# Performance work log

Measured on AMD Instinct MI355X. Metric: run time of the kernel, lower is better.

Reference implementation:

```python
import jax, jax.numpy as jnp
import numpy as np

NUM_CLASSES = 2
THRESHOLD = 0.35
NEGPOS_RATIO = 3
VAR0, VAR1 = 0.1, 0.2
ALPHA = 1.0
B, P, G = 16, 131072, 64


def _iou(a, b):
    # a: [G,4] point-form gts, b: [P,4] point-form priors -> [G,P]
    tl = jnp.maximum(a[:, None, :2], b[None, :, :2])
    br = jnp.minimum(a[:, None, 2:], b[None, :, 2:])
    wh = jnp.clip(br - tl, 0.0)
    inter = wh[..., 0] * wh[..., 1]
    area_a = (a[:, 2] - a[:, 0]) * (a[:, 3] - a[:, 1])
    area_b = (b[:, 2] - b[:, 0]) * (b[:, 3] - b[:, 1])
    return inter / (area_a[:, None] + area_b[None, :] - inter)


def setup_inputs() -> dict:
    key = jax.random.key(0)
    k1, k2, k3, k4, k5, k6 = jax.random.split(key, 6)
    loc_preds = jax.random.normal(k1, (B, P, 4), jnp.float32)
    cls_preds = jax.random.normal(k2, (B, P, NUM_CLASSES), jnp.float32)
    # priors in center form [cx, cy, w, h]
    pcxy = jax.random.uniform(k3, (P, 2), jnp.float32)
    pwh = 0.02 + 0.15 * jax.random.uniform(k4, (P, 2), jnp.float32)
    priorbox = jnp.concatenate([pcxy, pwh], axis=1)
    # ground-truth boxes; stored as [y1,x1,y2,x2,label] so that the module's
    # column permutation [1,0,3,2] yields valid point-form [x1,y1,x2,y2]
    xy1 = 0.8 * jax.random.uniform(k5, (B, G, 2), jnp.float32)
    wh = 0.02 + 0.1 * jax.random.uniform(k6, (B, G, 2), jnp.float32)
    xy2 = xy1 + wh
    boxes_perm = jnp.stack([xy1[..., 1], xy1[..., 0], xy2[..., 1], xy2[..., 0]], axis=-1)
    labels = jnp.ones((B, G, 1), jnp.float32)  # single foreground class (face)
    targets = jnp.concatenate([boxes_perm, labels], axis=-1)
    return {"loc_preds": loc_preds, "cls_preds": cls_preds,
            "priorbox": priorbox, "targets": targets}


def _loss(loc_preds, cls_preds, priorbox, targets):
    priors_c = priorbox[: loc_preds.shape[1], :]
    priors_pt = jnp.concatenate(
        [priors_c[:, :2] - priors_c[:, 2:] / 2,
         priors_c[:, :2] + priors_c[:, 2:] / 2], axis=1)
    num_g = targets.shape[1]

    def match_one(t):
        gts = t[:, :4][:, jnp.array([1, 0, 3, 2])]  # -> point form [x1,y1,x2,y2]
        labels = t[:, 4]
        ov = _iou(gts, priors_pt)                    # [G,P]
        best_prior_idx = jnp.argmax(ov, axis=1)      # [G]
        bto = jnp.max(ov, axis=0)                    # [P] best gt overlap per prior
        bti = jnp.argmax(ov, axis=0)                 # [P]
        bto = bto.at[best_prior_idx].set(2.0)        # force best prior per gt
        bti = bti.at[best_prior_idx].set(jnp.arange(num_g))
        conf = jnp.where(bto < THRESHOLD, 0.0, labels[bti])
        m = gts[bti]                                 # [P,4] matched gt boxes
        g_cxcy = ((m[:, :2] + m[:, 2:]) / 2 - priors_c[:, :2]) / (VAR0 * priors_c[:, 2:])
        g_wh = jnp.log((m[:, 2:] - m[:, :2]) / priors_c[:, 2:]) / VAR1
        return conf, jnp.concatenate([g_cxcy, g_wh], axis=1)

    cls_batch, loc_batch = jax.vmap(match_one)(targets)
    cls_batch = jax.lax.stop_gradient(cls_batch)   # targets require no grad
    loc_batch = jax.lax.stop_gradient(loc_batch)

    pos = cls_batch > 0                              # [B,P]
    npos = jnp.sum(pos)

    # smooth-L1 over positive priors, mean over selected elements (size_average)
    d = loc_preds - loc_batch
    ad = jnp.abs(d)
    sl1 = jnp.where(ad < 1.0, 0.5 * d * d, ad - 0.5)
    loss_loc = jnp.sum(sl1 * pos[..., None]) / jnp.maximum(npos * 4, 1).astype(sl1.dtype)

    # per-prior CE loss for hard-negative mining
    ignore = cls_batch < 0
    lbl = jnp.where(ignore, 0.0, cls_batch).astype(jnp.int32)
    lse = jax.nn.logsumexp(cls_preds, axis=-1)       # [B,P]
    gathered = jnp.take_along_axis(cls_preds, lbl[..., None], axis=-1)[..., 0]
    loss_c = jnp.where(pos | ignore, 0.0, lse - gathered)
    # two-stage sort: rank of each prior by descending loss
    loss_idx = jnp.argsort(-loss_c, axis=1)
    idx_rank = jnp.argsort(loss_idx, axis=1)
    num_pos_img = jnp.sum(pos, axis=1, keepdims=True)
    num_neg = jnp.minimum(NEGPOS_RATIO * num_pos_img, pos.shape[1] - 1)
    neg = idx_rank < num_neg
    mask = pos | neg
    # cross-entropy over mined samples, mean over selected (size_average)
    loss_cls = jnp.sum((lse - gathered) * mask) / jnp.maximum(jnp.sum(mask), 1).astype(lse.dtype)

    loss = (loss_cls + ALPHA * loss_loc) / npos.astype(lse.dtype)
    return loss, loss_loc, loss_cls


def reference(loc_preds, cls_preds, priorbox, targets):
    return _loss(loc_preds, cls_preds, priorbox, targets)
```

## Files before the change

### kernel.cpp

```cpp
#include <hip/hip_runtime.h>

#define BB 16
#define PP 131072
#define GG 64
#define THRESH 0.35f
#define RMAX 0.086f
#define NCHUNK 16
#define CPRIOR 8192

#define OFF_BESTP  0
#define OFF_H1C    131072
#define OFF_H1S    4325376
#define OFF_NPOSP  8519680
#define OFF_PCP    8520704
#define OFF_LOCP   8521728
#define OFF_CIDX   8522752
#define OFF_DONE   8522816
#define OFF_SELI   8522880
#define OFF_RESN   8523136
#define OFF_RESK   8523200
#define OFF_RESC   8523264
#define OFF_RESL   8523328
#define OFF_KEYS   8523392
#define OFF_BTO    16912000
#define OFF_BTI    25300608
#define OFF_CAND   27397760

__global__ __launch_bounds__(1024) void k_match(
    const float* __restrict__ priorbox, const float* __restrict__ targets,
    unsigned long long* __restrict__ bestp, float* __restrict__ bto,
    unsigned char* __restrict__ bti)
{
    __shared__ unsigned mlo[4096], mhi[4096];
    __shared__ float4 gxy[GG];
    __shared__ float gar[GG];
    __shared__ unsigned long long sbest[GG];
    const int b = blockIdx.y, chunk = blockIdx.x, tid = threadIdx.x;

    for (int i = tid; i < 4096; i += 1024) { mlo[i] = 0u; mhi[i] = 0u; }
    if (tid < GG) {
        const float* t = targets + (size_t)(b * GG + tid) * 5;
        float x1 = t[1], y1 = t[0], x2 = t[3], y2 = t[2];
        gxy[tid] = make_float4(x1, y1, x2, y2);
        gar[tid] = (x2 - x1) * (y2 - y1);
        sbest[tid] = 0ull;
    }
    __syncthreads();

    {
        const int g = tid & 63, strip = tid >> 6;
        float4 a = gxy[g];
        float ex1 = a.x - RMAX, ey1 = a.y - RMAX;
        float ex2 = a.z + RMAX, ey2 = a.w + RMAX;
        int cx0 = max(0, (int)(ex1 * 64.f));
        int cx1 = min(63, (int)ceilf(ex2 * 64.f) - 1);
        int cy0 = max(0, (int)(ey1 * 64.f));
        int cy1 = min(63, (int)ceilf(ey2 * 64.f) - 1);
        unsigned bit = 1u << (g & 31);
        unsigned* marr = (g < 32) ? mlo : mhi;
        for (int cy = cy0 + strip; cy <= cy1; cy += 16)
            for (int cx = cx0; cx <= cx1; cx++)
                atomicOr(&marr[cy * 64 + cx], bit);
    }
    __syncthreads();

#pragma unroll
    for (int j = 0; j < 8; j++) {
        const int p = chunk * CPRIOR + j * 1024 + tid;
        float4 pr = *reinterpret_cast<const float4*>(priorbox + (size_t)p * 4);
        float hx = 0.5f * pr.z, hy = 0.5f * pr.w;
        float px1 = pr.x - hx, py1 = pr.y - hy;
        float px2 = pr.x + hx, py2 = pr.y + hy;
        float par = (px2 - px1) * (py2 - py1);
        int cx = min(63, max(0, (int)(pr.x * 64.f)));
        int cy = min(63, max(0, (int)(pr.y * 64.f)));
        const int cell = cy * 64 + cx;
        unsigned m0 = mlo[cell], m1 = mhi[cell];
        const unsigned long long notp = (unsigned long long)(~(unsigned)p);
        float bv = -1.f; int bg = 0;
#pragma unroll 1
        for (int half = 0; half < 2; half++) {
            unsigned m = half ? m1 : m0;
            const int gbase = half ? 32 : 0;
            while (m) {
                const int g = gbase + __ffs(m) - 1;
                m &= m - 1;
                float4 a = gxy[g];
                float w = fminf(a.z, px2) - fmaxf(a.x, px1);
                float h = fminf(a.w, py2) - fmaxf(a.y, py1);
                w = fmaxf(w, 0.f); h = fmaxf(h, 0.f);
                float inter = w * h;
                float v = inter * __builtin_amdgcn_rcpf(gar[g] + par - inter);
                if (v > bv) { bv = v; bg = g; }
                if (v > 0.f) {
                    unsigned long long pk =
                        (((unsigned long long)__float_as_uint(v)) << 32) | notp;
                    atomicMax(&sbest[g], pk);
                }
            }
        }
        bto[(size_t)b * PP + p] = bv;
        bti[(size_t)b * PP + p] = (unsigned char)bg;
    }

    __syncthreads();
    if (tid < GG) bestp[(b * NCHUNK + chunk) * GG + tid] = sbest[tid];
}

__global__ __launch_bounds__(1024) void k_loss(
    const float* __restrict__ loc_preds, const float* __restrict__ cls_preds,
    const float* __restrict__ priorbox, const float* __restrict__ targets,
    const unsigned long long* __restrict__ bestp,
    const float* __restrict__ bto, const unsigned char* __restrict__ bti,
    unsigned* __restrict__ keys, unsigned* __restrict__ h1c, float* __restrict__ h1s,
    int* __restrict__ nposp, float* __restrict__ pcp, float* __restrict__ locp,
    unsigned* __restrict__ cidx, unsigned* __restrict__ done)
{
    __shared__ unsigned long long tmp64[1024];
    __shared__ unsigned hcnt[4096];
    __shared__ float hsum[4096];
    __shared__ float gx1[GG], gy1[GG], gx2[GG], gy2[GG], glab[GG];
    __shared__ unsigned blist[GG];
    __shared__ int nb;
    __shared__ float sred[32];
    __shared__ int sredi[16];
    const int b = blockIdx.y, chunk = blockIdx.x, tid = threadIdx.x;

    if (tid == 0 && chunk == 0) { cidx[b] = 0u; if (b == 0) *done = 0u; }

    tmp64[tid] = bestp[(b * NCHUNK + (tid >> 6)) * GG + (tid & 63)];
    for (int i = tid; i < 4096; i += 1024) { hcnt[i] = 0u; hsum[i] = 0.f; }
    if (tid < GG) {
        const float* t = targets + (size_t)(b * GG + tid) * 5;
        gx1[tid] = t[1]; gy1[tid] = t[0]; gx2[tid] = t[3]; gy2[tid] = t[2];
        glab[tid] = t[4];
    }
    __syncthreads();
    if (tid < GG) {
        unsigned long long m = tmp64[tid];
        for (int c = 1; c < NCHUNK; c++) {
            unsigned long long v = tmp64[c * GG + tid];
            m = v > m ? v : m;
        }
        tmp64[tid] = m;
    }
    __syncthreads();
    if (tid == 0) {
        int n = 0;
        for (int g = 0; g < GG; g++) {
            unsigned long long m = tmp64[g];
            if (m) {
                unsigned p = ~((unsigned)(m & 0xFFFFFFFFull));
                if ((int)(p >> 13) == chunk) blist[n++] = ((p & 8191u) << 6) | (unsigned)g;
            }
        }
        nb = n;
    }
    __syncthreads();

    const int nbl = nb;
    float locpart = 0.f, clspart = 0.f; int cnt = 0;
#pragma unroll
    for (int j = 0; j < 8; j++) {
        const int plocal = j * 1024 + tid;
        const size_t ip = (size_t)b * PP + chunk * CPRIOR + plocal;
        const float bv = bto[ip];
        int g = bti[ip];
        bool isb = false;
        for (int i = 0; i < nbl; i++) {
            unsigned e = blist[i];
            if ((int)(e >> 6) == plocal) { isb = true; g = (int)(e & 63u); }
        }
        const float2 cl = *reinterpret_cast<const float2*>(cls_preds + ip * 2);
        const float mx = fmaxf(cl.x, cl.y);
        const float lse = mx + log1pf(expf(fminf(cl.x, cl.y) - mx));
        const float conf = isb ? glab[g] : ((bv < THRESH) ? 0.f : glab[g]);
        unsigned key = 0u;
        if (conf > 0.f) {
            float gathered = (((int)conf) == 0) ? cl.x : cl.y;
            clspart += lse - gathered;
            cnt++;
            const int p = chunk * CPRIOR + plocal;
            float4 pr = *reinterpret_cast<const float4*>(priorbox + (size_t)p * 4);
            float mx1 = gx1[g], my1 = gy1[g], mx2 = gx2[g], my2 = gy2[g];
            float gcx = ((mx1 + mx2) * 0.5f - pr.x) / (0.1f * pr.z);
            float gcy = ((my1 + my2) * 0.5f - pr.y) / (0.1f * pr.w);
            float gw = logf((mx2 - mx1) / pr.z) / 0.2f;
            float gh = logf((my2 - my1) / pr.w) / 0.2f;
            float4 lp = *reinterpret_cast<const float4*>(loc_preds + ip * 4);
            float d0 = lp.x - gcx, d1 = lp.y - gcy, d2 = lp.z - gw, d3 = lp.w - gh;
            float a0 = fabsf(d0), a1 = fabsf(d1), a2 = fabsf(d2), a3 = fabsf(d3);
            locpart += ((a0 < 1.f) ? 0.5f * d0 * d0 : a0 - 0.5f)
                     + ((a1 < 1.f) ? 0.5f * d1 * d1 : a1 - 0.5f)
                     + ((a2 < 1.f) ? 0.5f * d2 * d2 : a2 - 0.5f)
                     + ((a3 < 1.f) ? 0.5f * d3 * d3 : a3 - 0.5f);
        } else {
            float lc = lse - cl.x;
            key = __float_as_uint(lc);
            atomicAdd(&hcnt[key >> 20], 1u);
            atomicAdd(&hsum[key >> 20], lc);
        }
        keys[ip] = key;
    }

    for (int o = 32; o; o >>= 1) {
        locpart += __shfl_xor(locpart, o);
        clspart += __shfl_xor(clspart, o);
        cnt     += __shfl_xor(cnt, o);
    }
    const int w = tid >> 6;
    if ((tid & 63) == 0) { sred[w] = locpart; sred[16 + w] = clspart; sredi[w] = cnt; }
    __syncthreads();
    if (tid == 0) {
        float l = 0.f, c = 0.f; int n = 0;
        for (int i = 0; i < 16; i++) { l += sred[i]; c += sred[16 + i]; n += sredi[i]; }
        nposp[b * NCHUNK + chunk] = n;
        pcp[b * NCHUNK + chunk] = c;
        locp[b * NCHUNK + chunk] = l;
    }
    __syncthreads();
    for (int i = tid; i < 4096; i += 1024) {
        h1c[(b * NCHUNK + chunk) * 4096 + i] = hcnt[i];
        h1s[(b * NCHUNK + chunk) * 4096 + i] = hsum[i];
    }
}

template <int NBINS>
__device__ void find_kth_par(const unsigned* __restrict__ h, int k, int* sel, int* krem)
{
    constexpr int PER = NBINS / 1024;
    __shared__ unsigned wsum_[16];
    __shared__ int res_[2];
    const int tid = threadIdx.x, lane = tid & 63, wid = tid >> 6;
    __syncthreads();
    unsigned own[PER];
    unsigned s = 0;
#pragma unroll
    for (int i = 0; i < PER; i++) { own[i] = h[NBINS - 1 - (tid * PER + i)]; s += own[i]; }
    unsigned incl = s;
    for (int d = 1; d < 64; d <<= 1) {
        unsigned t = __shfl_up(incl, d);
        if (lane >= d) incl += t;
    }
    if (lane == 63) wsum_[wid] = incl;
    if (tid == 0) { res_[0] = -1; res_[1] = 0; }
    __syncthreads();
    unsigned woff = 0;
    for (int w = 0; w < 16; w++) woff += (w < wid) ? wsum_[w] : 0u;
    const unsigned texcl = woff + incl - s;
    if (k > 0 && texcl < (unsigned)k && texcl + s >= (unsigned)k) {
        unsigned run = texcl;
#pragma unroll
        for (int i = 0; i < PER; i++) {
            run += own[i];
            if (run >= (unsigned)k) {
                res_[0] = NBINS - 1 - (tid * PER + i);
                res_[1] = k - (int)(run - own[i]);
                break;
            }
        }
    }
    __syncthreads();
    *sel = res_[0]; *krem = res_[1];
}

__device__ float block_sum_f(float v)
{
    __shared__ float rs[16];
    const int tid = threadIdx.x;
    __syncthreads();
    for (int o = 32; o; o >>= 1) v += __shfl_xor(v, o);
    if ((tid & 63) == 0) rs[tid >> 6] = v;
    __syncthreads();
    float s = 0.f;
    for (int i = 0; i < 16; i++) s += rs[i];
    return s;
}

__global__ __launch_bounds__(1024) void k_compact(
    const unsigned* __restrict__ keys, const unsigned* __restrict__ h1c,
    const int* __restrict__ nposp, unsigned* __restrict__ cand,
    unsigned* __restrict__ cidx, int* __restrict__ seli)
{
    __shared__ unsigned h1tot[4096];
    __shared__ int snp;
    __shared__ unsigned wcnt[16], wbase[16];
    __shared__ unsigned bbase;
    const int b = blockIdx.y, chunk = blockIdx.x, tid = threadIdx.x;
    const int lane = tid & 63, wid = tid >> 6;
    if (tid == 0) {
        int np = 0;
        for (int c = 0; c < NCHUNK; c++) np += nposp[b * NCHUNK + c];
        snp = np;
    }
    for (int i = tid; i < 4096; i += 1024) {
        unsigned s = 0;
        for (int c = 0; c < NCHUNK; c++) s += h1c[(b * NCHUNK + c) * 4096 + i];
        h1tot[i] = s;
    }
    unsigned kv[8];
#pragma unroll
    for (int j = 0; j < 8; j++)
        kv[j] = keys[(size_t)b * PP + chunk * CPRIOR + j * 1024 + tid];
    __syncthreads();
    const int np = snp;
    const int k = min(3 * np, PP - 1);
    int sel1, kk1;
    find_kth_par<4096>(h1tot, k, &sel1, &kk1);
    if (chunk == 0 && tid == 0) {
        seli[b * 4 + 0] = sel1; seli[b * 4 + 1] = kk1;
        seli[b * 4 + 2] = np;   seli[b * 4 + 3] = k;
    }
    const unsigned s1 = (unsigned)sel1;

    unsigned long long mv[8];
    unsigned wn = 0;
#pragma unroll
    for (int j = 0; j < 8; j++) {
        mv[j] = __ballot((kv[j] >> 20) == s1);
        wn += (unsigned)__popcll(mv[j]);
    }
    if (lane == 0) wcnt[wid] = wn;
    __syncthreads();
    if (tid == 0) {
        unsigned run = 0;
        for (int w = 0; w < 16; w++) { wbase[w] = run; run += wcnt[w]; }
        bbase = run ? atomicAdd(&cidx[b], run) : 0u;
    }
    __syncthreads();
    unsigned run = bbase + wbase[wid];
    const unsigned long long lanemask = (1ull << lane) - 1ull;
#pragma unroll
    for (int j = 0; j < 8; j++) {
        if ((kv[j] >> 20) == s1)
            cand[(size_t)b * PP + run + (unsigned)__popcll(mv[j] & lanemask)] = kv[j];
        run += (unsigned)__popcll(mv[j]);
    }
}

__global__ __launch_bounds__(1024) void k_select(
    const unsigned* __restrict__ cand, const unsigned* __restrict__ cidx,
    const float* __restrict__ h1s, const int* __restrict__ seli,
    const float* __restrict__ pcp, const float* __restrict__ locp,
    int* __restrict__ resn, int* __restrict__ resk,
    float* __restrict__ resc, float* __restrict__ resl,
    unsigned* __restrict__ done, float* __restrict__ out)
{
    __shared__ unsigned ch[1024];
    __shared__ float cs[1024];
    __shared__ int lastflag;
    const int b = blockIdx.x, tid = threadIdx.x;
    const int sel1 = seli[b * 4 + 0], kk1 = seli[b * 4 + 1];
    const int np   = seli[b * 4 + 2], k   = seli[b * 4 + 3];
    const unsigned ncand = cidx[b];

    float nh = 0.f;
    for (int i = tid * 4; i < tid * 4 + 4; i++) {
        if (i > sel1) {
            for (int c = 0; c < NCHUNK; c++) nh += h1s[(b * NCHUNK + c) * 4096 + i];
        }
    }
    float negsum_high = block_sum_f(nh);

    ch[tid] = 0u; cs[tid] = 0.f;
    __syncthreads();
    for (unsigned i = tid; i < ncand; i += 1024) {
        unsigned v = cand[(size_t)b * PP + i];
        unsigned bin = (v >> 10) & 1023u;
        atomicAdd(&ch[bin], 1u);
        atomicAdd(&cs[bin], __uint_as_float(v));
    }
    __syncthreads();
    int sel2, kk2;
    find_kth_par<1024>(ch, (sel1 < 0) ? 0 : kk1, &sel2, &kk2);
    float sumhi2 = block_sum_f((sel2 >= 0 && tid > sel2) ? cs[tid] : 0.f);

    __syncthreads();
    ch[tid] = 0u; cs[tid] = 0.f;
    __syncthreads();
    if (sel2 >= 0) {
        for (unsigned i = tid; i < ncand; i += 1024) {
            unsigned v = cand[(size_t)b * PP + i];
            if (((v >> 10) & 1023u) == (unsigned)sel2) {
                atomicAdd(&ch[v & 1023u], 1u);
                atomicAdd(&cs[v & 1023u], __uint_as_float(v));
            }
        }
    }
    __syncthreads();
    int sel3, needeq;
    find_kth_par<1024>(ch, (sel2 < 0) ? 0 : kk2, &sel3, &needeq);
    float sumhi3 = block_sum_f((sel3 >= 0 && tid > sel3) ? cs[tid] : 0.f);

    if (tid == 0) {
        float pcsum = 0.f, locsum = 0.f;
        for (int c = 0; c < NCHUNK; c++) {
            pcsum += pcp[b * NCHUNK + c];
            locsum += locp[b * NCHUNK + c];
        }
        float add = 0.f;
        if (sel3 >= 0 && needeq > 0) {
            unsigned Kstar = ((unsigned)sel1 << 20) | ((unsigned)sel2 << 10) | (unsigned)sel3;
            add = needeq * __uint_as_float(Kstar);
        }
        resn[b] = np;
        resk[b] = k;
        resc[b] = pcsum + negsum_high + sumhi2 + sumhi3 + add;
        resl[b] = locsum;
        __threadfence();
        unsigned old = atomicAdd(done, 1u);
        lastflag = (old == BB - 1) ? 1 : 0;
    }
    __syncthreads();
    if (!lastflag || tid != 0) return;

    __threadfence();
    volatile int* vrn = (volatile int*)resn;
    volatile int* vrk = (volatile int*)resk;
    volatile float* vrc = (volatile float*)resc;
    volatile float* vrl = (volatile float*)resl;
    int npt = 0; long long maskc = 0; float clsnum = 0.f, locnum = 0.f;
    for (int b2 = 0; b2 < BB; b2++) {
        npt += vrn[b2];
        maskc += (long long)vrn[b2] + vrk[b2];
        clsnum += vrc[b2];
        locnum += vrl[b2];
    }
    float denom_loc = (float)((4 * npt > 1) ? 4 * npt : 1);
    float denom_cls = (float)((maskc > 1) ? maskc : 1);
    float loss_loc = locnum / denom_loc;
    float loss_cls = clsnum / denom_cls;
    out[0] = (loss_cls + loss_loc) / (float)npt;
    out[1] = loss_loc;
    out[2] = loss_cls;
}

extern "C" void kernel_launch(void* const* d_in, const int* in_sizes, int n_in,
                              void* d_out, int out_size, void* d_ws, size_t ws_size,
                              hipStream_t stream)
{
    const float* loc_preds = (const float*)d_in[0];
    const float* cls_preds = (const float*)d_in[1];
    const float* priorbox  = (const float*)d_in[2];
    const float* targets   = (const float*)d_in[3];
    float* out = (float*)d_out;

    char* ws = (char*)d_ws;
    unsigned long long* bestp = (unsigned long long*)(ws + OFF_BESTP);
    unsigned* h1c    = (unsigned*)(ws + OFF_H1C);
    float*    h1s    = (float*)(ws + OFF_H1S);
    int*      nposp  = (int*)(ws + OFF_NPOSP);
    float*    pcp    = (float*)(ws + OFF_PCP);
    float*    locp   = (float*)(ws + OFF_LOCP);
    unsigned* cidx   = (unsigned*)(ws + OFF_CIDX);
    unsigned* done   = (unsigned*)(ws + OFF_DONE);
    int*      seli   = (int*)(ws + OFF_SELI);
    int*      resn   = (int*)(ws + OFF_RESN);
    int*      resk   = (int*)(ws + OFF_RESK);
    float*    resc   = (float*)(ws + OFF_RESC);
    float*    resl   = (float*)(ws + OFF_RESL);
    unsigned* keys   = (unsigned*)(ws + OFF_KEYS);
    float*    bto    = (float*)(ws + OFF_BTO);
    unsigned char* bti = (unsigned char*)(ws + OFF_BTI);
    unsigned* cand   = (unsigned*)(ws + OFF_CAND);

    k_match<<<dim3(NCHUNK, BB), 1024, 0, stream>>>(priorbox, targets, bestp, bto, bti);
    k_loss<<<dim3(NCHUNK, BB), 1024, 0, stream>>>(loc_preds, cls_preds, priorbox, targets,
                                                  bestp, bto, bti, keys, h1c, h1s,
                                                  nposp, pcp, locp, cidx, done);
    k_compact<<<dim3(NCHUNK, BB), 1024, 0, stream>>>(keys, h1c, nposp, cand, cidx, seli);
    k_select<<<BB, 1024, 0, stream>>>(cand, cidx, h1s, seli, pcp, locp,
                                      resn, resk, resc, resl, done, out);
}
```

Baseline: 113.2 us.

## Fuse match, loss, compact and select into one persistent kernel with per-image barriers

Merges the four kernels into a single launch of 256 blocks. Each image's 16 blocks synchronise through global atomic counters, and a small init kernel resets those counters. The best-overlap values, indices and keys now stay in registers instead of making round trips through global memory (bto/bti/keys), and the histogram totals are reduced in parallel across blocks. This removes launch gaps and global traffic, but it depends on all 16 blocks of an image being co-resident; otherwise the spin barriers can deadlock.

```diff
diff --git a/kernel.cpp b/kernel.cpp
--- a/kernel.cpp
+++ b/kernel.cpp
@@ -8,45 +8,140 @@
 #define NCHUNK 16
 #define CPRIOR 8192
 
-#define OFF_BESTP  0
-#define OFF_H1C    131072
-#define OFF_H1S    4325376
-#define OFF_NPOSP  8519680
-#define OFF_PCP    8520704
-#define OFF_LOCP   8521728
-#define OFF_CIDX   8522752
-#define OFF_DONE   8522816
-#define OFF_SELI   8522880
-#define OFF_RESN   8523136
-#define OFF_RESK   8523200
-#define OFF_RESC   8523264
-#define OFF_RESL   8523328
-#define OFF_KEYS   8523392
-#define OFF_BTO    16912000
-#define OFF_BTI    25300608
-#define OFF_CAND   27397760
-
-__global__ __launch_bounds__(1024) void k_match(
+#define OFF_BESTP   0
+#define OFF_H1C     131072
+#define OFF_H1S     4325376
+#define OFF_H1TOT   8519680
+#define OFF_H1STOT  8781824
+#define OFF_NPOSP   9043968
+#define OFF_PCP     9044992
+#define OFF_LOCP    9046016
+#define OFF_CIDX    9047040
+#define OFF_DONE    9047104
+#define OFF_BAR     9047168
+#define OFF_RESN    9047424
+#define OFF_RESK    9047488
+#define OFF_RESC    9047552
+#define OFF_RESL    9047616
+#define OFF_CAND    9047680
+
+__global__ void k_init(unsigned* __restrict__ cidx, unsigned* __restrict__ done,
+                       unsigned* __restrict__ bar)
+{
+    const int t = threadIdx.x;
+    if (t < BB) cidx[t] = 0u;
+    if (t == BB) *done = 0u;
+    if (t >= 32 && t < 32 + BB * 4) bar[t - 32] = 0u;
+}
+
+__device__ __forceinline__ void image_barrier(unsigned* ctr)
+{
+    __syncthreads();
+    if (threadIdx.x == 0) {
+        __threadfence();
+        atomicAdd(ctr, 1u);
+        while (atomicAdd(ctr, 0u) < NCHUNK)
+            __builtin_amdgcn_s_sleep(16);
+        __threadfence();
+    }
+    __syncthreads();
+}
+
+template <int NBINS>
+__device__ void find_kth_par(const unsigned* __restrict__ h, int k, int* sel, int* krem)
+{
+    constexpr int PER = NBINS / 1024;
+    __shared__ unsigned wsum_[16];
+    __shared__ int res_[2];
+    const int tid = threadIdx.x, lane = tid & 63, wid = tid >> 6;
+    __syncthreads();
+    unsigned own[PER];
+    unsigned s = 0;
+#pragma unroll
+    for (int i = 0; i < PER; i++) { own[i] = h[NBINS - 1 - (tid * PER + i)]; s += own[i]; }
+    unsigned incl = s;
+    for (int d = 1; d < 64; d <<= 1) {
+        unsigned t = __shfl_up(incl, d);
+        if (lane >= d) incl += t;
+    }
+    if (lane == 63) wsum_[wid] = incl;
+    if (tid == 0) { res_[0] = -1; res_[1] = 0; }
+    __syncthreads();
+    unsigned woff = 0;
+    for (int w = 0; w < 16; w++) woff += (w < wid) ? wsum_[w] : 0u;
+    const unsigned texcl = woff + incl - s;
+    if (k > 0 && texcl < (unsigned)k && texcl + s >= (unsigned)k) {
+        unsigned run = texcl;
+#pragma unroll
+        for (int i = 0; i < PER; i++) {
+            run += own[i];
+            if (run >= (unsigned)k) {
+                res_[0] = NBINS - 1 - (tid * PER + i);
+                res_[1] = k - (int)(run - own[i]);
+                break;
+            }
+        }
+    }
+    __syncthreads();
+    *sel = res_[0]; *krem = res_[1];
+}
+
+__device__ float block_sum_f(float v)
+{
+    __shared__ float rs[16];
+    const int tid = threadIdx.x;
+    __syncthreads();
+    for (int o = 32; o; o >>= 1) v += __shfl_xor(v, o);
+    if ((tid & 63) == 0) rs[tid >> 6] = v;
+    __syncthreads();
+    float s = 0.f;
+    for (int i = 0; i < 16; i++) s += rs[i];
+    return s;
+}
+
+__global__ __launch_bounds__(1024) void k_all(
+    const float* __restrict__ loc_preds, const float* __restrict__ cls_preds,
     const float* __restrict__ priorbox, const float* __restrict__ targets,
-    unsigned long long* __restrict__ bestp, float* __restrict__ bto,
-    unsigned char* __restrict__ bti)
-{
-    __shared__ unsigned mlo[4096], mhi[4096];
+    unsigned long long* __restrict__ bestp,
+    unsigned* __restrict__ h1c, float* __restrict__ h1s,
+    unsigned* __restrict__ h1tot, float* __restrict__ h1stot,
+    int* __restrict__ nposp, float* __restrict__ pcp, float* __restrict__ locp,
+    unsigned* __restrict__ cidx, unsigned* __restrict__ done, unsigned* __restrict__ bar,
+    int* __restrict__ resn, int* __restrict__ resk,
+    float* __restrict__ resc, float* __restrict__ resl,
+    unsigned* __restrict__ cand, float* __restrict__ out)
+{
     __shared__ float4 gxy[GG];
     __shared__ float gar[GG];
+    __shared__ float glab[GG];
     __shared__ unsigned long long sbest[GG];
+    __shared__ unsigned blist[GG];
+    __shared__ int nb;
+    __shared__ float sred[32];
+    __shared__ int sredi[16];
+    __shared__ unsigned wcnt[16], wbase[16];
+    __shared__ unsigned bbase;
+    __shared__ int lastflag;
+    __shared__ union SM {
+        struct { unsigned mlo[4096], mhi[4096]; } p1;
+        struct { unsigned long long tmp64[1024]; } p2a;
+        struct { unsigned hcnt[4096]; float hsum[4096]; } p2b;
+        struct { unsigned ch[1024]; float cs[1024]; } p4;
+    } U;
+
     const int b = blockIdx.y, chunk = blockIdx.x, tid = threadIdx.x;
-
-    for (int i = tid; i < 4096; i += 1024) { mlo[i] = 0u; mhi[i] = 0u; }
+    const int lane = tid & 63, wid = tid >> 6;
+
+    for (int i = tid; i < 4096; i += 1024) { U.p1.mlo[i] = 0u; U.p1.mhi[i] = 0u; }
     if (tid < GG) {
         const float* t = targets + (size_t)(b * GG + tid) * 5;
         float x1 = t[1], y1 = t[0], x2 = t[3], y2 = t[2];
         gxy[tid] = make_float4(x1, y1, x2, y2);
         gar[tid] = (x2 - x1) * (y2 - y1);
+        glab[tid] = t[4];
         sbest[tid] = 0ull;
     }
     __syncthreads();
-
     {
         const int g = tid & 63, strip = tid >> 6;
         float4 a = gxy[g];
@@ -57,13 +152,14 @@
         int cy0 = max(0, (int)(ey1 * 64.f));
         int cy1 = min(63, (int)ceilf(ey2 * 64.f) - 1);
         unsigned bit = 1u << (g & 31);
-        unsigned* marr = (g < 32) ? mlo : mhi;
+        unsigned* marr = (g < 32) ? U.p1.mlo : U.p1.mhi;
         for (int cy = cy0 + strip; cy <= cy1; cy += 16)
             for (int cx = cx0; cx <= cx1; cx++)
                 atomicOr(&marr[cy * 64 + cx], bit);
     }
     __syncthreads();
 
+    float bv[8]; int bg[8];
 #pragma unroll
     for (int j = 0; j < 8; j++) {
         const int p = chunk * CPRIOR + j * 1024 + tid;
@@ -75,9 +171,9 @@
         int cx = min(63, max(0, (int)(pr.x * 64.f)));
         int cy = min(63, max(0, (int)(pr.y * 64.f)));
         const int cell = cy * 64 + cx;
-        unsigned m0 = mlo[cell], m1 = mhi[cell];
+        unsigned m0 = U.p1.mlo[cell], m1 = U.p1.mhi[cell];
         const unsigned long long notp = (unsigned long long)(~(unsigned)p);
-        float bv = -1.f; int bg = 0;
+        float bvj = -1.f; int bgj = 0;
 #pragma unroll 1
         for (int half = 0; half < 2; half++) {
             unsigned m = half ? m1 : m0;
@@ -91,7 +187,7 @@
                 w = fmaxf(w, 0.f); h = fmaxf(h, 0.f);
                 float inter = w * h;
                 float v = inter * __builtin_amdgcn_rcpf(gar[g] + par - inter);
-                if (v > bv) { bv = v; bg = g; }
+                if (v > bvj) { bvj = v; bgj = g; }
                 if (v > 0.f) {
                     unsigned long long pk =
                         (((unsigned long long)__float_as_uint(v)) << 32) | notp;
@@ -99,56 +195,28 @@
                 }
             }
         }
-        bto[(size_t)b * PP + p] = bv;
-        bti[(size_t)b * PP + p] = (unsigned char)bg;
-    }
-
+        bv[j] = bvj; bg[j] = bgj;
+    }
     __syncthreads();
     if (tid < GG) bestp[(b * NCHUNK + chunk) * GG + tid] = sbest[tid];
-}
-
-__global__ __launch_bounds__(1024) void k_loss(
-    const float* __restrict__ loc_preds, const float* __restrict__ cls_preds,
-    const float* __restrict__ priorbox, const float* __restrict__ targets,
-    const unsigned long long* __restrict__ bestp,
-    const float* __restrict__ bto, const unsigned char* __restrict__ bti,
-    unsigned* __restrict__ keys, unsigned* __restrict__ h1c, float* __restrict__ h1s,
-    int* __restrict__ nposp, float* __restrict__ pcp, float* __restrict__ locp,
-    unsigned* __restrict__ cidx, unsigned* __restrict__ done)
-{
-    __shared__ unsigned long long tmp64[1024];
-    __shared__ unsigned hcnt[4096];
-    __shared__ float hsum[4096];
-    __shared__ float gx1[GG], gy1[GG], gx2[GG], gy2[GG], glab[GG];
-    __shared__ unsigned blist[GG];
-    __shared__ int nb;
-    __shared__ float sred[32];
-    __shared__ int sredi[16];
-    const int b = blockIdx.y, chunk = blockIdx.x, tid = threadIdx.x;
-
-    if (tid == 0 && chunk == 0) { cidx[b] = 0u; if (b == 0) *done = 0u; }
-
-    tmp64[tid] = bestp[(b * NCHUNK + (tid >> 6)) * GG + (tid & 63)];
-    for (int i = tid; i < 4096; i += 1024) { hcnt[i] = 0u; hsum[i] = 0.f; }
+
+    image_barrier(bar + b * 4 + 0);
+
+    U.p2a.tmp64[tid] = bestp[(b * NCHUNK + (tid >> 6)) * GG + (tid & 63)];
+    __syncthreads();
     if (tid < GG) {
-        const float* t = targets + (size_t)(b * GG + tid) * 5;
-        gx1[tid] = t[1]; gy1[tid] = t[0]; gx2[tid] = t[3]; gy2[tid] = t[2];
-        glab[tid] = t[4];
-    }
-    __syncthreads();
-    if (tid < GG) {
-        unsigned long long m = tmp64[tid];
+        unsigned long long m = U.p2a.tmp64[tid];
         for (int c = 1; c < NCHUNK; c++) {
-            unsigned long long v = tmp64[c * GG + tid];
+            unsigned long long v = U.p2a.tmp64[c * GG + tid];
             m = v > m ? v : m;
         }
-        tmp64[tid] = m;
+        U.p2a.tmp64[tid] = m;
     }
     __syncthreads();
     if (tid == 0) {
         int n = 0;
         for (int g = 0; g < GG; g++) {
-            unsigned long long m = tmp64[g];
+            unsigned long long m = U.p2a.tmp64[g];
             if (m) {
                 unsigned p = ~((unsigned)(m & 0xFFFFFFFFull));
                 if ((int)(p >> 13) == chunk) blist[n++] = ((p & 8191u) << 6) | (unsigned)g;
@@ -157,15 +225,17 @@
         nb = n;
     }
     __syncthreads();
-
     const int nbl = nb;
+    for (int i = tid; i < 4096; i += 1024) { U.p2b.hcnt[i] = 0u; U.p2b.hsum[i] = 0.f; }
+    __syncthreads();
+
+    unsigned kv[8];
     float locpart = 0.f, clspart = 0.f; int cnt = 0;
 #pragma unroll
     for (int j = 0; j < 8; j++) {
         const int plocal = j * 1024 + tid;
         const size_t ip = (size_t)b * PP + chunk * CPRIOR + plocal;
-        const float bv = bto[ip];
-        int g = bti[ip];
+        int g = bg[j];
         bool isb = false;
         for (int i = 0; i < nbl; i++) {
             unsigned e = blist[i];
@@ -174,7 +244,7 @@
         const float2 cl = *reinterpret_cast<const float2*>(cls_preds + ip * 2);
         const float mx = fmaxf(cl.x, cl.y);
         const float lse = mx + log1pf(expf(fminf(cl.x, cl.y) - mx));
-        const float conf = isb ? glab[g] : ((bv < THRESH) ? 0.f : glab[g]);
+        const float conf = isb ? glab[g] : ((bv[j] < THRESH) ? 0.f : glab[g]);
         unsigned key = 0u;
         if (conf > 0.f) {
             float gathered = (((int)conf) == 0) ? cl.x : cl.y;
@@ -182,11 +252,11 @@
             cnt++;
             const int p = chunk * CPRIOR + plocal;
             float4 pr = *reinterpret_cast<const float4*>(priorbox + (size_t)p * 4);
-            float mx1 = gx1[g], my1 = gy1[g], mx2 = gx2[g], my2 = gy2[g];
-            float gcx = ((mx1 + mx2) * 0.5f - pr.x) / (0.1f * pr.z);
-            float gcy = ((my1 + my2) * 0.5f - pr.y) / (0.1f * pr.w);
-            float gw = logf((mx2 - mx1) / pr.z) / 0.2f;
-            float gh = logf((my2 - my1) / pr.w) / 0.2f;
+            float4 gt = gxy[g];
+            float gcx = ((gt.x + gt.z) * 0.5f - pr.x) / (0.1f * pr.z);
+            float gcy = ((gt.y + gt.w) * 0.5f - pr.y) / (0.1f * pr.w);
+            float gw = logf((gt.z - gt.x) / pr.z) / 0.2f;
+            float gh = logf((gt.w - gt.y) / pr.w) / 0.2f;
             float4 lp = *reinterpret_cast<const float4*>(loc_preds + ip * 4);
             float d0 = lp.x - gcx, d1 = lp.y - gcy, d2 = lp.z - gw, d3 = lp.w - gh;
             float a0 = fabsf(d0), a1 = fabsf(d1), a2 = fabsf(d2), a3 = fabsf(d3);
@@ -197,10 +267,10 @@
         } else {
             float lc = lse - cl.x;
             key = __float_as_uint(lc);
-            atomicAdd(&hcnt[key >> 20], 1u);
-            atomicAdd(&hsum[key >> 20], lc);
-        }
-        keys[ip] = key;
+            atomicAdd(&U.p2b.hcnt[key >> 20], 1u);
+            atomicAdd(&U.p2b.hsum[key >> 20], lc);
+        }
+        kv[j] = key;
     }
 
     for (int o = 32; o; o >>= 1) {
@@ -208,8 +278,7 @@
         clspart += __shfl_xor(clspart, o);
         cnt     += __shfl_xor(cnt, o);
     }
-    const int w = tid >> 6;
-    if ((tid & 63) == 0) { sred[w] = locpart; sred[16 + w] = clspart; sredi[w] = cnt; }
+    if (lane == 0) { sred[wid] = locpart; sred[16 + wid] = clspart; sredi[wid] = cnt; }
     __syncthreads();
     if (tid == 0) {
         float l = 0.f, c = 0.f; int n = 0;
@@ -220,97 +289,31 @@
     }
     __syncthreads();
     for (int i = tid; i < 4096; i += 1024) {
-        h1c[(b * NCHUNK + chunk) * 4096 + i] = hcnt[i];
-        h1s[(b * NCHUNK + chunk) * 4096 + i] = hsum[i];
-    }
-}
-
-template <int NBINS>
-__device__ void find_kth_par(const unsigned* __restrict__ h, int k, int* sel, int* krem)
-{
-    constexpr int PER = NBINS / 1024;
-    __shared__ unsigned wsum_[16];
-    __shared__ int res_[2];
-    const int tid = threadIdx.x, lane = tid & 63, wid = tid >> 6;
-    __syncthreads();
-    unsigned own[PER];
-    unsigned s = 0;
-#pragma unroll
-    for (int i = 0; i < PER; i++) { own[i] = h[NBINS - 1 - (tid * PER + i)]; s += own[i]; }
-    unsigned incl = s;
-    for (int d = 1; d < 64; d <<= 1) {
-        unsigned t = __shfl_up(incl, d);
-        if (lane >= d) incl += t;
-    }
-    if (lane == 63) wsum_[wid] = incl;
-    if (tid == 0) { res_[0] = -1; res_[1] = 0; }
-    __syncthreads();
-    unsigned woff = 0;
-    for (int w = 0; w < 16; w++) woff += (w < wid) ? wsum_[w] : 0u;
-    const unsigned texcl = woff + incl - s;
-    if (k > 0 && texcl < (unsigned)k && texcl + s >= (unsigned)k) {
-        unsigned run = texcl;
-#pragma unroll
-        for (int i = 0; i < PER; i++) {
-            run += own[i];
-            if (run >= (unsigned)k) {
-                res_[0] = NBINS - 1 - (tid * PER + i);
-                res_[1] = k - (int)(run - own[i]);
-                break;
-            }
-        }
-    }
-    __syncthreads();
-    *sel = res_[0]; *krem = res_[1];
-}
-
-__device__ float block_sum_f(float v)
-{
-    __shared__ float rs[16];
-    const int tid = threadIdx.x;
-    __syncthreads();
-    for (int o = 32; o; o >>= 1) v += __shfl_xor(v, o);
-    if ((tid & 63) == 0) rs[tid >> 6] = v;
-    __syncthreads();
-    float s = 0.f;
-    for (int i = 0; i < 16; i++) s += rs[i];
-    return s;
-}
-
-__global__ __launch_bounds__(1024) void k_compact(
-    const unsigned* __restrict__ keys, const unsigned* __restrict__ h1c,
-    const int* __restrict__ nposp, unsigned* __restrict__ cand,
-    unsigned* __restrict__ cidx, int* __restrict__ seli)
-{
-    __shared__ unsigned h1tot[4096];
-    __shared__ int snp;
-    __shared__ unsigned wcnt[16], wbase[16];
-    __shared__ unsigned bbase;
-    const int b = blockIdx.y, chunk = blockIdx.x, tid = threadIdx.x;
-    const int lane = tid & 63, wid = tid >> 6;
-    if (tid == 0) {
-        int np = 0;
-        for (int c = 0; c < NCHUNK; c++) np += nposp[b * NCHUNK + c];
-        snp = np;
-    }
-    for (int i = tid; i < 4096; i += 1024) {
+        h1c[(b * NCHUNK + chunk) * 4096 + i] = U.p2b.hcnt[i];
+        h1s[(b * NCHUNK + chunk) * 4096 + i] = U.p2b.hsum[i];
+    }
+
+    image_barrier(bar + b * 4 + 1);
+
+    if (tid < 256) {
+        const int i = chunk * 256 + tid;
         unsigned s = 0;
-        for (int c = 0; c < NCHUNK; c++) s += h1c[(b * NCHUNK + c) * 4096 + i];
-        h1tot[i] = s;
-    }
-    unsigned kv[8];
-#pragma unroll
-    for (int j = 0; j < 8; j++)
-        kv[j] = keys[(size_t)b * PP + chunk * CPRIOR + j * 1024 + tid];
-    __syncthreads();
-    const int np = snp;
+        for (int cc = 0; cc < NCHUNK; cc++) s += h1c[(b * NCHUNK + cc) * 4096 + i];
+        h1tot[b * 4096 + i] = s;
+    } else if (tid < 512) {
+        const int i = chunk * 256 + (tid - 256);
+        float s = 0.f;
+        for (int cc = 0; cc < NCHUNK; cc++) s += h1s[(b * NCHUNK + cc) * 4096 + i];
+        h1stot[b * 4096 + i] = s;
+    }
+
+    image_barrier(bar + b * 4 + 2);
+
+    int np = 0;
+    for (int c = 0; c < NCHUNK; c++) np += nposp[b * NCHUNK + c];
     const int k = min(3 * np, PP - 1);
     int sel1, kk1;
-    find_kth_par<4096>(h1tot, k, &sel1, &kk1);
-    if (chunk == 0 && tid == 0) {
-        seli[b * 4 + 0] = sel1; seli[b * 4 + 1] = kk1;
-        seli[b * 4 + 2] = np;   seli[b * 4 + 3] = k;
-    }
+    find_kth_par<4096>(h1tot + b * 4096, k, &sel1, &kk1);
     const unsigned s1 = (unsigned)sel1;
 
     unsigned long long mv[8];
@@ -328,69 +331,57 @@
         bbase = run ? atomicAdd(&cidx[b], run) : 0u;
     }
     __syncthreads();
-    unsigned run = bbase + wbase[wid];
-    const unsigned long long lanemask = (1ull << lane) - 1ull;
-#pragma unroll
-    for (int j = 0; j < 8; j++) {
-        if ((kv[j] >> 20) == s1)
-            cand[(size_t)b * PP + run + (unsigned)__popcll(mv[j] & lanemask)] = kv[j];
-        run += (unsigned)__popcll(mv[j]);
-    }
-}
-
-__global__ __launch_bounds__(1024) void k_select(
-    const unsigned* __restrict__ cand, const unsigned* __restrict__ cidx,
-    const float* __restrict__ h1s, const int* __restrict__ seli,
-    const float* __restrict__ pcp, const float* __restrict__ locp,
-    int* __restrict__ resn, int* __restrict__ resk,
-    float* __restrict__ resc, float* __restrict__ resl,
-    unsigned* __restrict__ done, float* __restrict__ out)
-{
-    __shared__ unsigned ch[1024];
-    __shared__ float cs[1024];
-    __shared__ int lastflag;
-    const int b = blockIdx.x, tid = threadIdx.x;
-    const int sel1 = seli[b * 4 + 0], kk1 = seli[b * 4 + 1];
-    const int np   = seli[b * 4 + 2], k   = seli[b * 4 + 3];
+    {
+        unsigned run = bbase + wbase[wid];
+        const unsigned long long lanemask = (1ull << lane) - 1ull;
+#pragma unroll
+        for (int j = 0; j < 8; j++) {
+            if ((kv[j] >> 20) == s1)
+                cand[(size_t)b * PP + run + (unsigned)__popcll(mv[j] & lanemask)] = kv[j];
+            run += (unsigned)__popcll(mv[j]);
+        }
+    }
+
+    image_barrier(bar + b * 4 + 3);
+
+    if (chunk != 0) return;
+
     const unsigned ncand = cidx[b];
-
     float nh = 0.f;
-    for (int i = tid * 4; i < tid * 4 + 4; i++) {
-        if (i > sel1) {
-            for (int c = 0; c < NCHUNK; c++) nh += h1s[(b * NCHUNK + c) * 4096 + i];
-        }
-    }
+    for (int i = tid; i < 4096; i += 1024)
+        if (i > sel1) nh += h1stot[b * 4096 + i];
     float negsum_high = block_sum_f(nh);
 
-    ch[tid] = 0u; cs[tid] = 0.f;
+    __syncthreads();
+    U.p4.ch[tid] = 0u; U.p4.cs[tid] = 0.f;
     __syncthreads();
     for (unsigned i = tid; i < ncand; i += 1024) {
         unsigned v = cand[(size_t)b * PP + i];
         unsigned bin = (v >> 10) & 1023u;
-        atomicAdd(&ch[bin], 1u);
-        atomicAdd(&cs[bin], __uint_as_float(v));
+        atomicAdd(&U.p4.ch[bin], 1u);
+        atomicAdd(&U.p4.cs[bin], __uint_as_float(v));
     }
     __syncthreads();
     int sel2, kk2;
-    find_kth_par<1024>(ch, (sel1 < 0) ? 0 : kk1, &sel2, &kk2);
-    float sumhi2 = block_sum_f((sel2 >= 0 && tid > sel2) ? cs[tid] : 0.f);
-
-    __syncthreads();
-    ch[tid] = 0u; cs[tid] = 0.f;
+    find_kth_par<1024>(U.p4.ch, (sel1 < 0) ? 0 : kk1, &sel2, &kk2);
+    float sumhi2 = block_sum_f((sel2 >= 0 && tid > sel2) ? U.p4.cs[tid] : 0.f);
+
+    __syncthreads();
+    U.p4.ch[tid] = 0u; U.p4.cs[tid] = 0.f;
     __syncthreads();
     if (sel2 >= 0) {
         for (unsigned i = tid; i < ncand; i += 1024) {
             unsigned v = cand[(size_t)b * PP + i];
             if (((v >> 10) & 1023u) == (unsigned)sel2) {
-                atomicAdd(&ch[v & 1023u], 1u);
-                atomicAdd(&cs[v & 1023u], __uint_as_float(v));
+                atomicAdd(&U.p4.ch[v & 1023u], 1u);
+                atomicAdd(&U.p4.cs[v & 1023u], __uint_as_float(v));
             }
         }
     }
     __syncthreads();
     int sel3, needeq;
-    find_kth_par<1024>(ch, (sel2 < 0) ? 0 : kk2, &sel3, &needeq);
-    float sumhi3 = block_sum_f((sel3 >= 0 && tid > sel3) ? cs[tid] : 0.f);
+    find_kth_par<1024>(U.p4.ch, (sel2 < 0) ? 0 : kk2, &sel3, &needeq);
+    float sumhi3 = block_sum_f((sel3 >= 0 && tid > sel3) ? U.p4.cs[tid] : 0.f);
 
     if (tid == 0) {
         float pcsum = 0.f, locsum = 0.f;
@@ -449,26 +440,22 @@
     unsigned long long* bestp = (unsigned long long*)(ws + OFF_BESTP);
     unsigned* h1c    = (unsigned*)(ws + OFF_H1C);
     float*    h1s    = (float*)(ws + OFF_H1S);
+    unsigned* h1tot  = (unsigned*)(ws + OFF_H1TOT);
+    float*    h1stot = (float*)(ws + OFF_H1STOT);
     int*      nposp  = (int*)(ws + OFF_NPOSP);
     float*    pcp    = (float*)(ws + OFF_PCP);
     float*    locp   = (float*)(ws + OFF_LOCP);
     unsigned* cidx   = (unsigned*)(ws + OFF_CIDX);
     unsigned* done   = (unsigned*)(ws + OFF_DONE);
-    int*      seli   = (int*)(ws + OFF_SELI);
+    unsigned* bar    = (unsigned*)(ws + OFF_BAR);
     int*      resn   = (int*)(ws + OFF_RESN);
     int*      resk   = (int*)(ws + OFF_RESK);
     float*    resc   = (float*)(ws + OFF_RESC);
     float*    resl   = (float*)(ws + OFF_RESL);
-    unsigned* keys   = (unsigned*)(ws + OFF_KEYS);
-    float*    bto    = (float*)(ws + OFF_BTO);
-    unsigned char* bti = (unsigned char*)(ws + OFF_BTI);
     unsigned* cand   = (unsigned*)(ws + OFF_CAND);
 
-    k_match<<<dim3(NCHUNK, BB), 1024, 0, stream>>>(priorbox, targets, bestp, bto, bti);
-    k_loss<<<dim3(NCHUNK, BB), 1024, 0, stream>>>(loc_preds, cls_preds, priorbox, targets,
-                                                  bestp, bto, bti, keys, h1c, h1s,
-                                                  nposp, pcp, locp, cidx, done);
-    k_compact<<<dim3(NCHUNK, BB), 1024, 0, stream>>>(keys, h1c, nposp, cand, cidx, seli);
-    k_select<<<BB, 1024, 0, stream>>>(cand, cidx, h1s, seli, pcp, locp,
-                                      resn, resk, resc, resl, done, out);
-}
+    k_init<<<1, 128, 0, stream>>>(cidx, done, bar);
+    k_all<<<dim3(NCHUNK, BB), 1024, 0, stream>>>(
+        loc_preds, cls_preds, priorbox, targets, bestp, h1c, h1s, h1tot, h1stot,
+        nposp, pcp, locp, cidx, done, bar, resn, resk, resc, resl, cand, out);
+}
```

New measurement: 145.1 us. +28.1%, slower.
